# Kernel optimization log

Measured on AMD Instinct MI355X. Metric: run time of the kernel, lower is better.

Reference implementation:

```python
import jax, jax.numpy as jnp
import numpy as np

NMUL = 1
NEARZERO = 1e-5
ROUTING_LEN = 15
N_DYN = 3
N_STATIC = 13  # layout includes parRT, parAC (present in STATIC_PARAM_NAMES but unused in the step)


def _descale(x, lb, ub):
    return lb + x * (ub - lb)


def setup_inputs() -> dict:
    key = jax.random.key(0)
    k1, k2, k3 = jax.random.split(key, 3)
    T, G = 365, 50000
    u = jax.random.uniform(k1, (T, G, 3), dtype=jnp.float32)
    prcp = u[..., 0] * 10.0                 # mm/day
    tmean = (u[..., 1] - 0.3) * 20.0        # degC, roughly [-6, 14] so snow branch is exercised
    pet = u[..., 2] * 5.0                   # mm/day
    forcing = jnp.stack([prcp, tmean, pet], axis=-1)
    dyn_raw = jax.random.uniform(k2, (T, G, N_DYN * NMUL), dtype=jnp.float32)
    static_raw = jax.random.uniform(k3, (G, N_STATIC * NMUL + 2), dtype=jnp.float32)
    return {"forcing": forcing, "dyn_raw": dyn_raw, "static_raw": static_raw}


def _hbv_forward(forcing, dyn_raw, static_raw):
    T, G, _ = forcing.shape
    dt = forcing.dtype
    # --- descale dynamic params (per-timestep): parBETA, parK0, parBETAET ---
    dyn = dyn_raw.reshape(T, G, N_DYN, NMUL)
    parBETA = _descale(dyn[:, :, 0], 1.0, 6.0)
    parK0 = _descale(dyn[:, :, 1], 0.05, 0.9)
    parBETAET = _descale(dyn[:, :, 2], 0.3, 5.0)
    # --- descale static params ---
    st = static_raw[:, :N_STATIC * NMUL].reshape(G, N_STATIC, NMUL)
    parFC = _descale(st[:, 0], 50.0, 1000.0)
    parK1 = _descale(st[:, 1], 0.01, 0.5)
    parK2 = _descale(st[:, 2], 0.001, 0.2)
    parLP = _descale(st[:, 3], 0.2, 1.0)
    parPERC = _descale(st[:, 4], 0.0, 10.0)
    parUZL = _descale(st[:, 5], 0.0, 100.0)
    parTT = _descale(st[:, 6], -2.5, 2.5)
    parCFMAX = _descale(st[:, 7], 0.5, 10.0)
    parCFR = _descale(st[:, 8], 0.0, 0.1)
    parCWH = _descale(st[:, 9], 0.0, 0.2)
    parC = _descale(st[:, 10], 0.0, 1.0)
    rout = static_raw[:, N_STATIC * NMUL:]
    rout_a = _descale(rout[:, 0], 0.0, 2.9)
    rout_b = _descale(rout[:, 1], 0.0, 6.5)

    Pm = jnp.broadcast_to(forcing[..., 0:1], (T, G, NMUL))
    Tm = jnp.broadcast_to(forcing[..., 1:2], (T, G, NMUL))
    PETm = jnp.broadcast_to(forcing[..., 2:3], (T, G, NMUL))

    def step(carry, xs):
        SNOWPACK, MELTWATER, SM, SUZ, SLZ = carry
        PRECIP, TEMP, PET, pBETA, pK0, pBETAET = xs
        is_rain = (TEMP >= parTT).astype(dt)
        RAIN = PRECIP * is_rain
        SNOW = PRECIP * (1.0 - is_rain)
        SNOWPACK = SNOWPACK + SNOW
        melt = jnp.minimum(jnp.maximum(parCFMAX * (TEMP - parTT), 0.0), SNOWPACK)
        MELTWATER = MELTWATER + melt
        SNOWPACK = SNOWPACK - melt
        refreezing = jnp.minimum(jnp.maximum(parCFR * parCFMAX * (parTT - TEMP), 0.0), MELTWATER)
        SNOWPACK = SNOWPACK + refreezing
        MELTWATER = MELTWATER - refreezing
        tosoil = jnp.maximum(MELTWATER - parCWH * SNOWPACK, 0.0)
        MELTWATER = MELTWATER - tosoil
        soil_wetness = jnp.clip((SM / parFC) ** pBETA, 0.0, 1.0)
        recharge = (RAIN + tosoil) * soil_wetness
        SM = SM + RAIN + tosoil - recharge
        excess = jnp.maximum(SM - parFC, 0.0)
        SM = SM - excess
        evapfactor = jnp.clip((SM / (parLP * parFC)) ** pBETAET, 0.0, 1.0)
        ETact = jnp.minimum(SM, PET * evapfactor)
        SM = jnp.maximum(SM - ETact, NEARZERO)
        capillary = jnp.minimum(SLZ, parC * SLZ * (1.0 - jnp.minimum(SM / parFC, 1.0)))
        SM = jnp.maximum(SM + capillary, NEARZERO)
        SLZ = jnp.maximum(SLZ - capillary, NEARZERO)
        SUZ = SUZ + recharge + excess
        PERC = jnp.minimum(SUZ, parPERC)
        SUZ = SUZ - PERC
        Q0 = pK0 * jnp.maximum(SUZ - parUZL, 0.0)
        SUZ = SUZ - Q0
        Q1 = parK1 * SUZ
        SUZ = SUZ - Q1
        SLZ = jnp.maximum(SLZ + PERC, 0.0)
        Q2 = parK2 * SLZ
        SLZ = SLZ - Q2
        return (SNOWPACK, MELTWATER, SM, SUZ, SLZ), Q0 + Q1 + Q2

    init = tuple(jnp.full((G, NMUL), 0.001, dtype=dt) for _ in range(5))
    _, Qall = jax.lax.scan(step, init, (Pm, Tm, PETm, parBETA, parK0, parBETAET))
    Qsim = Qall.mean(axis=-1)  # [T, G]: average over nmul components

    # --- gamma unit-hydrograph routing (hydroDL UH_gamma + causal conv, lenF = 15) ---
    aa = jax.nn.relu(rout_a) + 0.1      # shape param, [G]
    theta = jax.nn.relu(rout_b) + 0.5   # scale param, [G]
    t = jnp.arange(0.5, ROUTING_LEN, dtype=dt)[:, None]  # [15, 1] midpoints
    w = (t ** (aa - 1.0)) * jnp.exp(-t / theta) / (jnp.exp(jax.lax.lgamma(aa)) * theta ** aa)
    w = w / w.sum(axis=0)  # [15, G], normalized UH weights
    Qpad = jnp.pad(Qsim, ((ROUTING_LEN - 1, 0), (0, 0)))
    # causal conv: Qrout[t] = sum_k w[k] * Qsim[t-k]; fixed 15-tap loop
    Qrout = sum(w[k] * jax.lax.dynamic_slice_in_dim(Qpad, ROUTING_LEN - 1 - k, T, axis=0)
                for k in range(ROUTING_LEN))
    return Qrout  # streamflow [T, G]


def reference(forcing, dyn_raw, static_raw):
    return _hbv_forward(forcing, dyn_raw, static_raw)
```

## Files before the change

### kernel.cpp

```cpp
#include <hip/hip_runtime.h>

#define NEARZERO 1e-5f
#define RLEN 15
#define LOG2E 1.4426950408889634f

struct __attribute__((packed, aligned(4))) F3 { float x, y, z; };
static __device__ __forceinline__ F3 ldo(const char* base, unsigned voff) {
    return *reinterpret_cast<const F3*>(base + voff);
}

struct Par { float FC, invFC, invLPFC, K1, K2, PERC, UZL, TT, CFMAX, CFRC, CWH, C; };

__device__ __forceinline__ void ab_step(
    const F3& f, const F3& d3, const Par& pr,
    float& SP, float& MW, float& SM, float& SLZ,
    float cs, float& rxP, float& k0P)
{
    const float pBETA   = fmaf(d3.x, 5.0f, 1.0f);
    const float pBETAET = fmaf(d3.z, 4.7f, 0.3f);
    const float dT   = f.y - pr.TT;
    const float RAIN = (dT >= 0.0f) ? f.x : 0.0f;
    SP += f.x - RAIN;
    const float melt = __builtin_amdgcn_fmed3f(pr.CFMAX * dT, 0.0f, SP);
    MW += melt;  SP -= melt;
    const float refr = __builtin_amdgcn_fmed3f(pr.CFRC * (0.0f - dT), 0.0f, MW);
    SP += refr;  MW -= refr;
    const float tosoil = fmaxf(fmaf(-pr.CWH, SP, MW), 0.0f);
    MW -= tosoil;
    const float sw = fminf(exp2f(pBETA * __log2f(SM * pr.invFC)), 1.0f);
    const float rt = RAIN + tosoil;
    const float rc = rt * sw;
    SM = fmaf(rt, 1.0f - sw, SM);
    const float ex = fmaxf(SM - pr.FC, 0.0f);
    SM = fminf(SM, pr.FC);
    const float ef = fminf(exp2f(pBETAET * __log2f(SM * pr.invLPFC)), 1.0f);
    SM = fmaxf(SM - f.z * ef, NEARZERO);
    const float cap = cs * (1.0f - fminf(SM * pr.invFC, 1.0f));
    SM  = fmaxf(SM + cap, NEARZERO);
    SLZ = fmaxf(SLZ - cap, NEARZERO);
    rxP = rc + ex;
    k0P = fmaf(d3.y, 0.85f, 0.05f);
}

template<int PH>
__device__ __forceinline__ void fused_iter(
    const F3 f, const F3 d3, const Par& pr,
    float& SP, float& MW, float& SM, float& SUZ, float& SLZ,
    float& rxP, float& k0P,
    float (&acc)[RLEN], const float (&w)[RLEN],
    float* outp, bool guard)
{
    const float t1 = __log2f(SM * pr.invFC);
    const float dT   = f.y - pr.TT;
    const float RAIN = (dT >= 0.0f) ? f.x : 0.0f;
    SP += f.x - RAIN;
    const float melt = __builtin_amdgcn_fmed3f(pr.CFMAX * dT, 0.0f, SP);
    MW += melt;  SP -= melt;
    const float refr = __builtin_amdgcn_fmed3f(pr.CFRC * (0.0f - dT), 0.0f, MW);
    SP += refr;  MW -= refr;
    const float tosoil = fmaxf(fmaf(-pr.CWH, SP, MW), 0.0f);
    MW -= tosoil;
    SUZ += rxP;
    const float PERCv = fminf(SUZ, pr.PERC);
    SUZ -= PERCv;
    const float Q0 = k0P * fmaxf(SUZ - pr.UZL, 0.0f);
    SUZ -= Q0;
    const float Q1 = pr.K1 * SUZ;
    SUZ -= Q1;
    const float pBETA = fmaf(d3.x, 5.0f, 1.0f);
    const float sw = fminf(exp2f(pBETA * t1), 1.0f);
    const float rt = RAIN + tosoil;
    SLZ += PERCv;
    const float Q2 = pr.K2 * SLZ;
    SLZ -= Q2;
    const float Qs = Q0 + Q1 + Q2;
    const float cs = pr.C * SLZ;
    const float rc = rt * sw;
    SM = fmaf(rt, 1.0f - sw, SM);
    const float ex = fmaxf(SM - pr.FC, 0.0f);
    SM = fminf(SM, pr.FC);
    const float t2 = __log2f(SM * pr.invLPFC);
    const float qr = fmaf(w[0], Qs, acc[PH]);
    acc[PH] = 0.0f;
#pragma unroll
    for (int k = 1; k < RLEN; ++k) {
        const int j = (PH + k) % RLEN;
        acc[j] = fmaf(w[k], Qs, acc[j]);
    }
    if (guard) __builtin_nontemporal_store(qr, outp);
    const float pBETAET = fmaf(d3.z, 4.7f, 0.3f);
    const float ef = fminf(exp2f(pBETAET * t2), 1.0f);
    SM = fmaxf(SM - f.z * ef, NEARZERO);
    const float cap = cs * (1.0f - fminf(SM * pr.invFC, 1.0f));
    SM  = fmaxf(SM + cap, NEARZERO);
    SLZ = fmaxf(SLZ - cap, NEARZERO);
    rxP = rc + ex;
    k0P = fmaf(d3.y, 0.85f, 0.05f);
}

template<int PH>
__device__ __forceinline__ void finish_step(
    const Par& pr, float& SUZ, float& SLZ, float rxP, float k0P,
    float (&acc)[RLEN], const float (&w)[RLEN], float* outp, bool guard)
{
    SUZ += rxP;
    const float PERCv = fminf(SUZ, pr.PERC);
    SUZ -= PERCv;
    const float Q0 = k0P * fmaxf(SUZ - pr.UZL, 0.0f);
    SUZ -= Q0;
    const float Q1 = pr.K1 * SUZ;
    SUZ -= Q1;
    SLZ += PERCv;
    const float Q2 = pr.K2 * SLZ;
    SLZ -= Q2;
    const float Qs = Q0 + Q1 + Q2;
    const float qr = fmaf(w[0], Qs, acc[PH]);
    if (guard) __builtin_nontemporal_store(qr, outp);
}

__global__ __launch_bounds__(256, 1)
void hbv_kernel(const float* __restrict__ forcing,
                const float* __restrict__ dynr,
                const float* __restrict__ statr,
                float* __restrict__ out,
                int G)
{
    const int g  = blockIdx.x * 256 + threadIdx.x;
    const int gc = (g < G) ? g : (G - 1);
    const bool guard = (g < G);

    const float* sp = statr + (size_t)gc * 15;
    Par pr;
    pr.FC    = fmaf(sp[0], 950.0f, 50.0f);
    pr.K1    = fmaf(sp[1], 0.49f, 0.01f);
    pr.K2    = fmaf(sp[2], 0.199f, 0.001f);
    const float parLP = fmaf(sp[3], 0.8f, 0.2f);
    pr.PERC  = sp[4] * 10.0f;
    pr.UZL   = sp[5] * 100.0f;
    pr.TT    = fmaf(sp[6], 5.0f, -2.5f);
    pr.CFMAX = fmaf(sp[7], 9.5f, 0.5f);
    pr.CFRC  = (sp[8] * 0.1f) * pr.CFMAX;
    pr.CWH   = sp[9] * 0.2f;
    pr.C     = sp[10];
    const float rout_a = sp[13] * 2.9f;
    const float rout_b = sp[14] * 6.5f;
    pr.invFC   = 1.0f / pr.FC;
    pr.invLPFC = 1.0f / (parLP * pr.FC);

    const float aa    = fmaxf(rout_a, 0.0f) + 0.1f;
    const float theta = fmaxf(rout_b, 0.0f) + 0.5f;
    const float am1   = aa - 1.0f;
    const float nitl2 = -LOG2E / theta;
    float w[RLEN];
    float wsum = 0.0f;
#pragma unroll
    for (int k = 0; k < RLEN; ++k) {
        const float tk = (float)k + 0.5f;
        w[k] = exp2f(am1 * __log2f(tk) + tk * nitl2);
        wsum += w[k];
    }
    const float winv = 1.0f / wsum;
#pragma unroll
    for (int k = 0; k < RLEN; ++k) w[k] *= winv;

    float SP_ = 0.001f, MW = 0.001f, SM = 0.001f, SUZ = 0.001f, SLZ = 0.001f;
    float acc[RLEN];
#pragma unroll
    for (int k = 0; k < RLEN; ++k) acc[k] = 0.0f;
    float rxP = 0.0f, k0P = 0.0f;

    const char* fbase = (const char*)forcing;
    const char* dbase = (const char*)dynr;
    char*       obase = (char*)out;
    const unsigned G12 = (unsigned)G * 12u;
    const unsigned G4  = (unsigned)G * 4u;
    unsigned vRun = (unsigned)gc * 12u;
    unsigned vO   = (unsigned)g  * 4u;

    F3 bF[5], bD[5];
#pragma unroll
    for (int r = 0; r < 5; ++r) {
        bF[r] = ldo(fbase, vRun); bD[r] = ldo(dbase, vRun);
        vRun += G12;
    }

    {
        const float cs0 = pr.C * SLZ;
        const F3 f_ = bF[0], d_ = bD[0];
        bF[0] = ldo(fbase, vRun); bD[0] = ldo(dbase, vRun);
        vRun += G12;
        __builtin_amdgcn_sched_barrier(0x7);
        ab_step(f_, d_, pr, SP_, MW, SM, SLZ, cs0, rxP, k0P);
    }

#define ITER(MM, VOFF) do { \
    constexpr int PH_ = (MM) % RLEN; \
    constexpr int S_  = ((MM) + 1) % 5; \
    const F3 f_ = bF[S_], d_ = bD[S_]; \
    bF[S_] = ldo(fbase, (VOFF)); bD[S_] = ldo(dbase, (VOFF)); \
    __builtin_amdgcn_sched_barrier(0x7); \
    fused_iter<PH_>(f_, d_, pr, SP_, MW, SM, SUZ, SLZ, rxP, k0P, acc, w, \
                    (float*)(obase + vO), guard); \
    vO += G4; \
} while (0)

#define ITERADV(MM) do { ITER(MM, vRun); vRun += G12; } while (0)

#define ITER_NL(MM) do { \
    constexpr int PH_ = (MM) % RLEN; \
    constexpr int S_  = ((MM) + 1) % 5; \
    const F3 f_ = bF[S_], d_ = bD[S_]; \
    fused_iter<PH_>(f_, d_, pr, SP_, MW, SM, SUZ, SLZ, rxP, k0P, acc, w, \
                    (float*)(obase + vO), guard); \
    vO += G4; \
} while (0)

    for (int i = 0; i < 23; ++i) {
        ITERADV(0);  ITERADV(1);  ITERADV(2);  ITERADV(3);  ITERADV(4);
        ITERADV(5);  ITERADV(6);  ITERADV(7);  ITERADV(8);  ITERADV(9);
        ITERADV(10); ITERADV(11); ITERADV(12); ITERADV(13); ITERADV(14);
    }
    ITERADV(0);  ITERADV(1);  ITERADV(2);  ITERADV(3);  ITERADV(4);
    ITERADV(5);  ITERADV(6);  ITERADV(7);  ITERADV(8);  ITERADV(9);
    ITERADV(10); ITERADV(11); ITERADV(12); ITERADV(13);
    ITER(14, (unsigned)gc * 12u + 364u * G12);
    ITER_NL(0); ITER_NL(1); ITER_NL(2); ITER_NL(3);
    finish_step<4>(pr, SUZ, SLZ, rxP, k0P, acc, w, (float*)(obase + vO), guard);
#undef ITER_NL
#undef ITERADV
#undef ITER
}

extern "C" void kernel_launch(void* const* d_in, const int* in_sizes, int n_in,
                              void* d_out, int out_size, void* d_ws, size_t ws_size,
                              hipStream_t stream) {
    const float* forcing = (const float*)d_in[0];
    const float* dynr    = (const float*)d_in[1];
    const float* statr   = (const float*)d_in[2];
    float* out = (float*)d_out;

    const int G = in_sizes[2] / 15;
    const int block = 256;
    const int grid  = (G + block - 1) / block;
    hbv_kernel<<<grid, block, 0, stream>>>(forcing, dynr, statr, out, G);
}
```

Before: 97.81 us.

## Shrink prefetch depth to three, early-exit out-of-range threads, fold negations into params

Cuts the register prefetch ring for forcing and dynamic parameters from five steps to three. Threads past G now return early instead of clamping their index and guarding stores. Sign flips are folded into precomputed refreeze and water-holding constants, and several expressions are rewritten as FMAs with shorter dependency chains. The shallower prefetch frees registers but hides less memory latency in a kernel that streams its inputs.

```diff
diff --git a/kernel.cpp b/kernel.cpp
--- a/kernel.cpp
+++ b/kernel.cpp
@@ -9,33 +9,33 @@
     return *reinterpret_cast<const F3*>(base + voff);
 }
 
-struct Par { float FC, invFC, invLPFC, K1, K2, PERC, UZL, TT, CFMAX, CFRC, CWH, C; };
+struct Par { float FC, invFC, invLPFC, K1, K2, PERC, UZL, TT, CFMAX, nCFRC, nCWH, C; };
 
 __device__ __forceinline__ void ab_step(
     const F3& f, const F3& d3, const Par& pr,
     float& SP, float& MW, float& SM, float& SLZ,
     float cs, float& rxP, float& k0P)
 {
-    const float pBETA   = fmaf(d3.x, 5.0f, 1.0f);
-    const float pBETAET = fmaf(d3.z, 4.7f, 0.3f);
     const float dT   = f.y - pr.TT;
-    const float RAIN = (dT >= 0.0f) ? f.x : 0.0f;
-    SP += f.x - RAIN;
+    const float SNOW = (dT >= 0.0f) ? 0.0f : f.x;
+    const float RAIN = f.x - SNOW;
+    SP += SNOW;
     const float melt = __builtin_amdgcn_fmed3f(pr.CFMAX * dT, 0.0f, SP);
     MW += melt;  SP -= melt;
-    const float refr = __builtin_amdgcn_fmed3f(pr.CFRC * (0.0f - dT), 0.0f, MW);
+    const float refr = __builtin_amdgcn_fmed3f(pr.nCFRC * dT, 0.0f, MW);
     SP += refr;  MW -= refr;
-    const float tosoil = fmaxf(fmaf(-pr.CWH, SP, MW), 0.0f);
+    const float tosoil = fmaxf(fmaf(pr.nCWH, SP, MW), 0.0f);
     MW -= tosoil;
-    const float sw = fminf(exp2f(pBETA * __log2f(SM * pr.invFC)), 1.0f);
+    const float sw = fminf(exp2f(fmaf(d3.x, 5.0f, 1.0f) * __log2f(SM * pr.invFC)), 1.0f);
     const float rt = RAIN + tosoil;
     const float rc = rt * sw;
     SM = fmaf(rt, 1.0f - sw, SM);
     const float ex = fmaxf(SM - pr.FC, 0.0f);
     SM = fminf(SM, pr.FC);
-    const float ef = fminf(exp2f(pBETAET * __log2f(SM * pr.invLPFC)), 1.0f);
-    SM = fmaxf(SM - f.z * ef, NEARZERO);
-    const float cap = cs * (1.0f - fminf(SM * pr.invFC, 1.0f));
+    const float ef = fminf(exp2f(fmaf(d3.z, 4.7f, 0.3f) * __log2f(SM * pr.invLPFC)), 1.0f);
+    SM = fmaxf(fmaf(-f.z, ef, SM), NEARZERO);
+    const float u  = fminf(SM * pr.invFC, 1.0f);
+    const float cap = fmaf(-cs, u, cs);
     SM  = fmaxf(SM + cap, NEARZERO);
     SLZ = fmaxf(SLZ - cap, NEARZERO);
     rxP = rc + ex;
@@ -48,33 +48,33 @@
     float& SP, float& MW, float& SM, float& SUZ, float& SLZ,
     float& rxP, float& k0P,
     float (&acc)[RLEN], const float (&w)[RLEN],
-    float* outp, bool guard)
+    float* outp)
 {
     const float t1 = __log2f(SM * pr.invFC);
     const float dT   = f.y - pr.TT;
-    const float RAIN = (dT >= 0.0f) ? f.x : 0.0f;
-    SP += f.x - RAIN;
+    const float SNOW = (dT >= 0.0f) ? 0.0f : f.x;
+    const float RAIN = f.x - SNOW;
+    SP += SNOW;
     const float melt = __builtin_amdgcn_fmed3f(pr.CFMAX * dT, 0.0f, SP);
     MW += melt;  SP -= melt;
-    const float refr = __builtin_amdgcn_fmed3f(pr.CFRC * (0.0f - dT), 0.0f, MW);
+    const float refr = __builtin_amdgcn_fmed3f(pr.nCFRC * dT, 0.0f, MW);
     SP += refr;  MW -= refr;
-    const float tosoil = fmaxf(fmaf(-pr.CWH, SP, MW), 0.0f);
+    const float tosoil = fmaxf(fmaf(pr.nCWH, SP, MW), 0.0f);
     MW -= tosoil;
-    SUZ += rxP;
-    const float PERCv = fminf(SUZ, pr.PERC);
-    SUZ -= PERCv;
-    const float Q0 = k0P * fmaxf(SUZ - pr.UZL, 0.0f);
-    SUZ -= Q0;
-    const float Q1 = pr.K1 * SUZ;
-    SUZ -= Q1;
-    const float pBETA = fmaf(d3.x, 5.0f, 1.0f);
-    const float sw = fminf(exp2f(pBETA * t1), 1.0f);
+    const float a  = SUZ + rxP;
+    const float PERCv = fminf(a, pr.PERC);
+    const float b  = a - PERCv;
+    const float Q0 = k0P * fmaxf(b - pr.UZL, 0.0f);
+    const float c  = b - Q0;
+    const float Q1 = pr.K1 * c;
+    SUZ = c - Q1;
+    const float sw = fminf(exp2f(fmaf(d3.x, 5.0f, 1.0f) * t1), 1.0f);
     const float rt = RAIN + tosoil;
-    SLZ += PERCv;
-    const float Q2 = pr.K2 * SLZ;
-    SLZ -= Q2;
-    const float Qs = Q0 + Q1 + Q2;
+    const float dz = SLZ + PERCv;
+    const float Q2 = pr.K2 * dz;
+    SLZ = dz - Q2;
     const float cs = pr.C * SLZ;
+    const float Qs = (Q0 + Q1) + Q2;
     const float rc = rt * sw;
     SM = fmaf(rt, 1.0f - sw, SM);
     const float ex = fmaxf(SM - pr.FC, 0.0f);
@@ -87,11 +87,11 @@
         const int j = (PH + k) % RLEN;
         acc[j] = fmaf(w[k], Qs, acc[j]);
     }
-    if (guard) __builtin_nontemporal_store(qr, outp);
-    const float pBETAET = fmaf(d3.z, 4.7f, 0.3f);
-    const float ef = fminf(exp2f(pBETAET * t2), 1.0f);
-    SM = fmaxf(SM - f.z * ef, NEARZERO);
-    const float cap = cs * (1.0f - fminf(SM * pr.invFC, 1.0f));
+    __builtin_nontemporal_store(qr, outp);
+    const float ef = fminf(exp2f(fmaf(d3.z, 4.7f, 0.3f) * t2), 1.0f);
+    SM = fmaxf(fmaf(-f.z, ef, SM), NEARZERO);
+    const float u  = fminf(SM * pr.invFC, 1.0f);
+    const float cap = fmaf(-cs, u, cs);
     SM  = fmaxf(SM + cap, NEARZERO);
     SLZ = fmaxf(SLZ - cap, NEARZERO);
     rxP = rc + ex;
@@ -99,23 +99,21 @@
 }
 
 template<int PH>
-__device__ __forceinline__ void finish_step(
+__device__ __forceinline__ void finish_last(
     const Par& pr, float& SUZ, float& SLZ, float rxP, float k0P,
-    float (&acc)[RLEN], const float (&w)[RLEN], float* outp, bool guard)
-{
-    SUZ += rxP;
-    const float PERCv = fminf(SUZ, pr.PERC);
-    SUZ -= PERCv;
-    const float Q0 = k0P * fmaxf(SUZ - pr.UZL, 0.0f);
-    SUZ -= Q0;
-    const float Q1 = pr.K1 * SUZ;
-    SUZ -= Q1;
-    SLZ += PERCv;
-    const float Q2 = pr.K2 * SLZ;
-    SLZ -= Q2;
-    const float Qs = Q0 + Q1 + Q2;
+    float (&acc)[RLEN], const float (&w)[RLEN], float* outp)
+{
+    const float a  = SUZ + rxP;
+    const float PERCv = fminf(a, pr.PERC);
+    const float b  = a - PERCv;
+    const float Q0 = k0P * fmaxf(b - pr.UZL, 0.0f);
+    const float c  = b - Q0;
+    const float Q1 = pr.K1 * c;
+    const float dz = SLZ + PERCv;
+    const float Q2 = pr.K2 * dz;
+    const float Qs = (Q0 + Q1) + Q2;
     const float qr = fmaf(w[0], Qs, acc[PH]);
-    if (guard) __builtin_nontemporal_store(qr, outp);
+    __builtin_nontemporal_store(qr, outp);
 }
 
 __global__ __launch_bounds__(256, 1)
@@ -125,11 +123,10 @@
                 float* __restrict__ out,
                 int G)
 {
-    const int g  = blockIdx.x * 256 + threadIdx.x;
-    const int gc = (g < G) ? g : (G - 1);
-    const bool guard = (g < G);
-
-    const float* sp = statr + (size_t)gc * 15;
+    const int g = blockIdx.x * 256 + threadIdx.x;
+    if (g >= G) return;
+
+    const float* sp = statr + (size_t)g * 15;
     Par pr;
     pr.FC    = fmaf(sp[0], 950.0f, 50.0f);
     pr.K1    = fmaf(sp[1], 0.49f, 0.01f);
@@ -139,8 +136,8 @@
     pr.UZL   = sp[5] * 100.0f;
     pr.TT    = fmaf(sp[6], 5.0f, -2.5f);
     pr.CFMAX = fmaf(sp[7], 9.5f, 0.5f);
-    pr.CFRC  = (sp[8] * 0.1f) * pr.CFMAX;
-    pr.CWH   = sp[9] * 0.2f;
+    pr.nCFRC = -(sp[8] * 0.1f) * pr.CFMAX;
+    pr.nCWH  = -(sp[9] * 0.2f);
     pr.C     = sp[10];
     const float rout_a = sp[13] * 2.9f;
     const float rout_b = sp[14] * 6.5f;
@@ -174,12 +171,12 @@
     char*       obase = (char*)out;
     const unsigned G12 = (unsigned)G * 12u;
     const unsigned G4  = (unsigned)G * 4u;
-    unsigned vRun = (unsigned)gc * 12u;
-    unsigned vO   = (unsigned)g  * 4u;
-
-    F3 bF[5], bD[5];
-#pragma unroll
-    for (int r = 0; r < 5; ++r) {
+    unsigned vRun = (unsigned)g * 12u;
+    unsigned vO   = (unsigned)g * 4u;
+
+    F3 bF[3], bD[3];
+#pragma unroll
+    for (int r = 0; r < 3; ++r) {
         bF[r] = ldo(fbase, vRun); bD[r] = ldo(dbase, vRun);
         vRun += G12;
     }
@@ -193,41 +190,30 @@
         ab_step(f_, d_, pr, SP_, MW, SM, SLZ, cs0, rxP, k0P);
     }
 
-#define ITER(MM, VOFF) do { \
+#define ITER(MM, DOLOAD) do { \
     constexpr int PH_ = (MM) % RLEN; \
-    constexpr int S_  = ((MM) + 1) % 5; \
+    constexpr int S_  = ((MM) + 1) % 3; \
     const F3 f_ = bF[S_], d_ = bD[S_]; \
-    bF[S_] = ldo(fbase, (VOFF)); bD[S_] = ldo(dbase, (VOFF)); \
+    if (DOLOAD) { \
+        bF[S_] = ldo(fbase, vRun); bD[S_] = ldo(dbase, vRun); \
+        vRun += G12; \
+    } \
     __builtin_amdgcn_sched_barrier(0x7); \
     fused_iter<PH_>(f_, d_, pr, SP_, MW, SM, SUZ, SLZ, rxP, k0P, acc, w, \
-                    (float*)(obase + vO), guard); \
+                    (float*)(obase + vO)); \
     vO += G4; \
 } while (0)
 
-#define ITERADV(MM) do { ITER(MM, vRun); vRun += G12; } while (0)
-
-#define ITER_NL(MM) do { \
-    constexpr int PH_ = (MM) % RLEN; \
-    constexpr int S_  = ((MM) + 1) % 5; \
-    const F3 f_ = bF[S_], d_ = bD[S_]; \
-    fused_iter<PH_>(f_, d_, pr, SP_, MW, SM, SUZ, SLZ, rxP, k0P, acc, w, \
-                    (float*)(obase + vO), guard); \
-    vO += G4; \
-} while (0)
-
-    for (int i = 0; i < 23; ++i) {
-        ITERADV(0);  ITERADV(1);  ITERADV(2);  ITERADV(3);  ITERADV(4);
-        ITERADV(5);  ITERADV(6);  ITERADV(7);  ITERADV(8);  ITERADV(9);
-        ITERADV(10); ITERADV(11); ITERADV(12); ITERADV(13); ITERADV(14);
-    }
-    ITERADV(0);  ITERADV(1);  ITERADV(2);  ITERADV(3);  ITERADV(4);
-    ITERADV(5);  ITERADV(6);  ITERADV(7);  ITERADV(8);  ITERADV(9);
-    ITERADV(10); ITERADV(11); ITERADV(12); ITERADV(13);
-    ITER(14, (unsigned)gc * 12u + 364u * G12);
-    ITER_NL(0); ITER_NL(1); ITER_NL(2); ITER_NL(3);
-    finish_step<4>(pr, SUZ, SLZ, rxP, k0P, acc, w, (float*)(obase + vO), guard);
-#undef ITER_NL
-#undef ITERADV
+    for (int i = 0; i < 24; ++i) {
+        ITER(0, true);  ITER(1, true);  ITER(2, true);  ITER(3, true);  ITER(4, true);
+        ITER(5, true);  ITER(6, true);  ITER(7, true);  ITER(8, true);  ITER(9, true);
+        ITER(10, true); ITER(11, true); ITER(12, true); ITER(13, true); ITER(14, true);
+    }
+    ITER(0, true);
+    ITER(1, false);
+    ITER(2, false);
+    ITER(3, false);
+    finish_last<4>(pr, SUZ, SLZ, rxP, k0P, acc, w, (float*)(obase + vO));
 #undef ITER
 }
 
```

After: 115.4 us, median of 2. 1.18x slower.
